# Kernel tuning notes

Measured on AMD Instinct MI355X. Metric: run time of the kernel, lower is better.

The kernel has to match this reference:

```python
import jax, jax.numpy as jnp
import numpy as np

B, C, H, W = 8, 64, 64, 64
T, G, HID = 8, 8, 64


def setup_inputs() -> dict:
    key = jax.random.key(0)
    ks = jax.random.split(key, 8)
    s = 0.05
    return {
        "h": jax.random.normal(ks[0], (B, C, H, W), jnp.float32),
        "w_in": jax.random.normal(ks[1], (G * T, C), jnp.float32) * s,
        "b_in": jnp.zeros((G * T,), jnp.float32),
        "w_ih": jax.random.normal(ks[2], (4 * HID, 1), jnp.float32) * s,
        "w_hh": jax.random.normal(ks[3], (4 * HID, HID), jnp.float32) * s,
        "b_ih": jnp.zeros((4 * HID,), jnp.float32),
        "b_hh": jnp.zeros((4 * HID,), jnp.float32),
        "w_s": jax.random.normal(ks[4], (1, HID), jnp.float32) * s,
        "b_s": jnp.zeros((1,), jnp.float32),
        "w_out": jax.random.normal(ks[5], (C, G * T), jnp.float32) * s,
        "b_out": jnp.zeros((C,), jnp.float32),
    }


def reference(h, w_in, b_in, w_ih, w_hh, b_ih, b_hh, w_s, b_s, w_out, b_out):
    Bb, Cc, Hh, Ww = h.shape
    # 1x1 conv in-projection: (B,C,H,W) -> (B,G*T,H,W)
    y = jnp.einsum('bchw,oc->bohw', h, w_in) + b_in[None, :, None, None]
    y = y.reshape(Bb, G, T, Hh, Ww)
    # (B,G,H,W,T) -> (N,T) scalar sequences
    seq = jnp.transpose(y, (0, 1, 3, 4, 2)).reshape(-1, T)
    N = seq.shape[0]
    xs = seq.T  # (T, N) time-major for scan
    bias = b_ih + b_hh  # (4H,)
    w_x = w_ih[:, 0]    # (4H,) scalar-input weights

    def step(carry, x_t):
        hprev, cprev = carry
        # gates: i, f, g, o in torch LSTM ordering
        gates = x_t[:, None] * w_x[None, :] + hprev @ w_hh.T + bias  # (N,4H)
        i, f, g, o = jnp.split(gates, 4, axis=1)
        i = jax.nn.sigmoid(i)
        f = jax.nn.sigmoid(f)
        o = jax.nn.sigmoid(o)
        g = jnp.tanh(g)
        c = f * cprev + i * g
        hn = o * jnp.tanh(c)
        s_t = hn @ w_s[0] + b_s[0]  # fused to_scalar: (N,)
        return (hn, c), s_t

    init = (jnp.zeros((N, HID), h.dtype), jnp.zeros((N, HID), h.dtype))
    _, s = jax.lax.scan(step, init, xs)  # s: (T, N)

    out = s.T.reshape(Bb, G, Hh, Ww, T)
    out = jnp.transpose(out, (0, 1, 4, 2, 3)).reshape(Bb, G * T, Hh, Ww)
    # 1x1 conv out-projection back to C channels
    out = jnp.einsum('bchw,oc->bohw', out, w_out) + b_out[None, :, None, None]
    return out
```

## Files before the change

### kernel.cpp

```cpp
#include <hip/hip_runtime.h>
#include <hip/hip_bf16.h>

#define HW    4096
#define BB    8
#define TT    8

constexpr int OFF_WFRAG = 0;
constexpr int OFF_WTOUT = OFF_WFRAG + 8704;
constexpr int OFF_WXB   = OFF_WTOUT + 4096;

constexpr float SI = -1.44269504088896340736f;
constexpr float SG =  2.88539008177792681472f;

typedef _Float16 halfx8 __attribute__((ext_vector_type(8)));
typedef float    floatx4 __attribute__((ext_vector_type(4)));
typedef float    floatx2 __attribute__((ext_vector_type(2)));

__device__ inline float fast_exp2(float x) {
#if __has_builtin(__builtin_amdgcn_exp2f)
    return __builtin_amdgcn_exp2f(x);
#else
    return __builtin_exp2f(x);
#endif
}
__device__ inline float fast_rcp(float x) {
#if __has_builtin(__builtin_amdgcn_rcpf)
    return __builtin_amdgcn_rcpf(x);
#else
    return 1.0f / x;
#endif
}
__device__ inline floatx2 exp2x2(floatx2 x) {
    floatx2 r; r.x = fast_exp2(x.x); r.y = fast_exp2(x.y); return r;
}
__device__ inline floatx2 rcpx2(floatx2 x) {
    floatx2 r; r.x = fast_rcp(x.x); r.y = fast_rcp(x.y); return r;
}

union pack8 { _Float16 h[8]; uint4 u; };

__global__ __launch_bounds__(256) void prep_kernel(
    const float* __restrict__ w_ih,  const float* __restrict__ w_hh,
    const float* __restrict__ b_ih,  const float* __restrict__ b_hh,
    const float* __restrict__ w_s,   const float* __restrict__ w_out,
    float* __restrict__ ws_f) {
    int tid = threadIdx.x;
    int bid = blockIdx.x;
    if (bid < 9) {
        int e = bid * 256 + tid;
        uint4* wf = (uint4*)(ws_f + OFF_WFRAG);
        if (e < 2048) {
            int l  = e & 63;
            int fi = e >> 6;
            int nb = fi >> 1, kc = fi & 1;
            int gate = (l & 15) + 16 * nb;
            int hid  = kc * 32 + (l >> 4) * 8;
            float sc = (gate >= 128 && gate < 192) ? SG : SI;
            const float* src = w_hh + gate * 64 + hid;
            pack8 p;
            #pragma unroll
            for (int j = 0; j < 8; ++j) p.h[j] = (_Float16)(src[j] * sc);
            wf[e] = p.u;
        } else if (e < 2176) {
            int t2 = e - 2048;
            int l = t2 & 63, kc = t2 >> 6;
            pack8 p;
            #pragma unroll
            for (int j = 0; j < 8; ++j) p.h[j] = (_Float16)0.0f;
            if ((l & 15) == 0) {
                #pragma unroll
                for (int j = 0; j < 8; ++j)
                    p.h[j] = (_Float16)w_s[kc * 32 + (l >> 4) * 8 + j];
            }
            wf[e] = p.u;
        }
    } else if (bid == 9) {
        floatx2* wxb = (floatx2*)(ws_f + OFF_WXB);
        float sc = (tid >= 128 && tid < 192) ? SG : SI;
        floatx2 v; v.x = w_ih[tid] * sc; v.y = (b_ih[tid] + b_hh[tid]) * sc;
        wxb[tid] = v;
    } else {
        #pragma unroll
        for (int i = 0; i < 8; ++i) {
            int idx = (bid - 10) * 2048 + tid + 256 * i;
            int o = idx & 63, c = idx >> 6;
            ws_f[OFF_WTOUT + idx] = w_out[o * 64 + c];
        }
    }
}

__global__ __launch_bounds__(512) void lstm_kernel(
    const float* __restrict__ hin,
    const float* __restrict__ ws_f,
    float* __restrict__ out,
    const float* __restrict__ w_in,
    const float* __restrict__ b_in,
    const float* __restrict__ b_s_p,
    const float* __restrict__ b_out) {
    __shared__ uint4 wfrag_lds[2176];
    __shared__ floatx2 wxb_lds[256];
    __shared__ __align__(16) float x_lds[1024];
    __shared__ __align__(16) _Float16 h_lds[9216];
    __shared__ __align__(16) float stile[1024];
    __shared__ __align__(16) float wt_lds[4096];

    int tid = threadIdx.x;
    int ptile = blockIdx.x & 255;
    int b     = blockIdx.x >> 8;
    int p0 = ptile * 16;

    int lane = tid & 63;
    int wv   = tid >> 6;
    int g    = wv;
    int s    = lane & 15;
    int q    = lane >> 4;

    const uint4* wfg = (const uint4*)(ws_f + OFF_WFRAG);
    #pragma unroll
    for (int i = 0; i < 5; ++i) {
        int e = tid + 512 * i;
        if (e < 2176) wfrag_lds[e] = wfg[e];
    }
    if (tid < 256) wxb_lds[tid] = ((const floatx2*)(ws_f + OFF_WXB))[tid];
    #pragma unroll
    for (int i = 0; i < 2; ++i)
        ((floatx4*)wt_lds)[tid + 512 * i] = ((const floatx4*)w_in)[tid + 512 * i];
    if (tid < 256) {
        int cc = tid >> 2, f4 = tid & 3;
        ((floatx4*)stile)[tid] = *(const floatx4*)&hin[(b * 64 + cc) * HW + p0 + f4 * 4];
    }
    __syncthreads();

    {
        floatx2 xacc; xacc.x = b_in[g * 8 + q]; xacc.y = b_in[g * 8 + q + 4];
        #pragma unroll 8
        for (int cc = 0; cc < 64; ++cc) {
            float hv = stile[cc * 16 + s];
            floatx2 w;
            w.x = wt_lds[(g * 8 + q) * 64 + cc];
            w.y = wt_lds[(g * 8 + q + 4) * 64 + cc];
            floatx2 h2; h2.x = hv; h2.y = hv;
            xacc = xacc + w * h2;
        }
        x_lds[g * 128 + q * 16 + s]       = xacc.x;
        x_lds[g * 128 + (q + 4) * 16 + s] = xacc.y;
    }
    #pragma unroll
    for (int i = 0; i < 9; ++i)
        ((unsigned*)h_lds)[tid + 512 * i] = 0u;
    __syncthreads();

    #pragma unroll
    for (int i = 0; i < 2; ++i)
        ((floatx4*)wt_lds)[tid + 512 * i] =
            ((const floatx4*)(ws_f + OFF_WTOUT))[tid + 512 * i];

    _Float16* hrow = h_lds + wv * 16 * 72;
    float bs = b_s_p[0];

    float c_st[4][4];
    #pragma unroll
    for (int hb = 0; hb < 4; ++hb)
        #pragma unroll
        for (int r = 0; r < 4; ++r) c_st[hb][r] = 0.0f;

    for (int t = 0; t < TT; ++t) {
        asm volatile("" ::: "memory");

        halfx8 a0 = *(const halfx8*)(hrow + s * 72 + q * 8);
        halfx8 a1 = *(const halfx8*)(hrow + s * 72 + q * 8 + 32);

        if (t > 0) {
            halfx8 sb0 = *(const halfx8*)&wfrag_lds[32 * 64 + lane];
            halfx8 sb1 = *(const halfx8*)&wfrag_lds[33 * 64 + lane];
            floatx4 sa = {0.f, 0.f, 0.f, 0.f};
            sa = __builtin_amdgcn_mfma_f32_16x16x32_f16(a0, sb0, sa, 0, 0, 0);
            sa = __builtin_amdgcn_mfma_f32_16x16x32_f16(a1, sb1, sa, 0, 0, 0);
            if (s == 0) {
                floatx4 o4 = {sa[0] + bs, sa[1] + bs, sa[2] + bs, sa[3] + bs};
                *(floatx4*)&stile[(g * 8 + (t - 1)) * 16 + q * 4] = o4;
            }
        }

        floatx4 xv = *(const floatx4*)&x_lds[g * 128 + t * 16 + q * 4];
        floatx2 xlo; xlo.x = xv[0]; xlo.y = xv[1];
        floatx2 xhi; xhi.x = xv[2]; xhi.y = xv[3];

        #pragma unroll
        for (int hb = 0; hb < 4; ++hb) {
            floatx4 acc[4];
            #pragma unroll
            for (int gi = 0; gi < 4; ++gi) {
                int nb = hb + 4 * gi;
                floatx2 wb = wxb_lds[s + 16 * nb];
                floatx2 lo = xlo * wb.x + wb.y;
                floatx2 hi = xhi * wb.x + wb.y;
                floatx4 a = {lo.x, lo.y, hi.x, hi.y};
                halfx8 b0 = *(const halfx8*)&wfrag_lds[(nb * 2 + 0) * 64 + lane];
                halfx8 b1 = *(const halfx8*)&wfrag_lds[(nb * 2 + 1) * 64 + lane];
                a = __builtin_amdgcn_mfma_f32_16x16x32_f16(a0, b0, a, 0, 0, 0);
                a = __builtin_amdgcn_mfma_f32_16x16x32_f16(a1, b1, a, 0, 0, 0);
                acc[gi] = a;
            }
            int s16 = s + 16 * hb;
            _Float16* wp = hrow + (q * 4) * 72 + s16;
            #pragma unroll
            for (int p = 0; p < 2; ++p) {
                int r0 = 2 * p;
                floatx2 Ei; Ei.x = fast_exp2(acc[0][r0]); Ei.y = fast_exp2(acc[0][r0 + 1]);
                floatx2 Ef; Ef.x = fast_exp2(acc[1][r0]); Ef.y = fast_exp2(acc[1][r0 + 1]);
                floatx2 Eg; Eg.x = fast_exp2(acc[2][r0]); Eg.y = fast_exp2(acc[2][r0 + 1]);
                floatx2 Eo; Eo.x = fast_exp2(acc[3][r0]); Eo.y = fast_exp2(acc[3][r0 + 1]);
                floatx2 Bf  = Ef + 1.0f;
                floatx2 Pig = (Ei + 1.0f) * (Eg + 1.0f);
                floatx2 cp; cp.x = c_st[hb][r0]; cp.y = c_st[hb][r0 + 1];
                floatx2 num = cp * Pig + (Eg * SG - SG) * Bf;
                floatx2 cs  = num * rcpx2(Bf * Pig);
                c_st[hb][r0] = cs.x; c_st[hb][r0 + 1] = cs.y;
                floatx2 Ec  = exp2x2(cs);
                floatx2 hn  = (Ec - 1.0f) * rcpx2((Eo + 1.0f) * (Ec + 1.0f));
                wp[(r0 + 0) * 72] = (_Float16)hn.x;
                wp[(r0 + 1) * 72] = (_Float16)hn.y;
            }
        }
    }
    {
        asm volatile("" ::: "memory");
        halfx8 a0 = *(const halfx8*)(hrow + s * 72 + q * 8);
        halfx8 a1 = *(const halfx8*)(hrow + s * 72 + q * 8 + 32);
        halfx8 sb0 = *(const halfx8*)&wfrag_lds[32 * 64 + lane];
        halfx8 sb1 = *(const halfx8*)&wfrag_lds[33 * 64 + lane];
        floatx4 sa = {0.f, 0.f, 0.f, 0.f};
        sa = __builtin_amdgcn_mfma_f32_16x16x32_f16(a0, sb0, sa, 0, 0, 0);
        sa = __builtin_amdgcn_mfma_f32_16x16x32_f16(a1, sb1, sa, 0, 0, 0);
        if (s == 0) {
            floatx4 o4 = {sa[0] + bs, sa[1] + bs, sa[2] + bs, sa[3] + bs};
            *(floatx4*)&stile[(g * 8 + 7) * 16 + q * 4] = o4;
        }
    }
    __syncthreads();

    {
        int px = tid & 15;
        int oo = tid >> 4;
        floatx2 acc; acc.x = b_out[oo]; acc.y = b_out[oo + 32];
        #pragma unroll 8
        for (int c = 0; c < 64; ++c) {
            float sv = stile[c * 16 + px];
            floatx2 w;
            w.x = wt_lds[c * 64 + oo];
            w.y = wt_lds[c * 64 + oo + 32];
            floatx2 s2; s2.x = sv; s2.y = sv;
            acc = acc + w * s2;
        }
        out[(b * 64 + oo) * HW + p0 + px]      = acc.x;
        out[(b * 64 + oo + 32) * HW + p0 + px] = acc.y;
    }
}

extern "C" void kernel_launch(void* const* d_in, const int* in_sizes, int n_in,
                              void* d_out, int out_size, void* d_ws, size_t ws_size,
                              hipStream_t stream) {
    const float* h     = (const float*)d_in[0];
    const float* w_in  = (const float*)d_in[1];
    const float* b_in  = (const float*)d_in[2];
    const float* w_ih  = (const float*)d_in[3];
    const float* w_hh  = (const float*)d_in[4];
    const float* b_ih  = (const float*)d_in[5];
    const float* b_hh  = (const float*)d_in[6];
    const float* w_s   = (const float*)d_in[7];
    const float* b_s   = (const float*)d_in[8];
    const float* w_out = (const float*)d_in[9];
    const float* b_out = (const float*)d_in[10];
    float* out = (float*)d_out;
    float* ws  = (float*)d_ws;

    prep_kernel<<<12, 256, 0, stream>>>(w_ih, w_hh, b_ih, b_hh, w_s, w_out, ws);
    lstm_kernel<<<2048, 512, 0, stream>>>(h, ws, out, w_in, b_in, b_s, b_out);
}
```

Before: 232.7 us.

## Permute LSTM gate layout for packed h stores, hoist weights, vectorize out-projection

The recurrent weight fragments and input/bias table are permuted in the prep kernel so that each lane owns four consecutive hidden units. The new h state can then be written to LDS as halfx4 vectors instead of scalar half stores. The per-gate input weights and the to_scalar fragments are hoisted into registers outside the time loop. The out-projection now reads w_out untransposed with floatx4 LDS loads, which removes the transpose pass from the prep kernel. A min-blocks launch bound is added; it may force a tight register budget and cause spills, given the extra register-resident weights.

```diff
diff --git a/kernel.cpp b/kernel.cpp
--- a/kernel.cpp
+++ b/kernel.cpp
@@ -6,13 +6,13 @@
 #define TT    8
 
 constexpr int OFF_WFRAG = 0;
-constexpr int OFF_WTOUT = OFF_WFRAG + 8704;
-constexpr int OFF_WXB   = OFF_WTOUT + 4096;
+constexpr int OFF_WXB   = 12800;
 
 constexpr float SI = -1.44269504088896340736f;
 constexpr float SG =  2.88539008177792681472f;
 
 typedef _Float16 halfx8 __attribute__((ext_vector_type(8)));
+typedef _Float16 halfx4 __attribute__((ext_vector_type(4)));
 typedef float    floatx4 __attribute__((ext_vector_type(4)));
 typedef float    floatx2 __attribute__((ext_vector_type(2)));
 
@@ -53,9 +53,10 @@
             int l  = e & 63;
             int fi = e >> 6;
             int nb = fi >> 1, kc = fi & 1;
-            int gate = (l & 15) + 16 * nb;
+            int hb = nb & 3, gi = nb >> 2;
+            int gate = gi * 64 + 4 * (l & 15) + hb;
             int hid  = kc * 32 + (l >> 4) * 8;
-            float sc = (gate >= 128 && gate < 192) ? SG : SI;
+            float sc = (gi == 2) ? SG : SI;
             const float* src = w_hh + gate * 64 + hid;
             pack8 p;
             #pragma unroll
@@ -74,29 +75,24 @@
             }
             wf[e] = p.u;
         }
-    } else if (bid == 9) {
-        floatx2* wxb = (floatx2*)(ws_f + OFF_WXB);
-        float sc = (tid >= 128 && tid < 192) ? SG : SI;
-        floatx2 v; v.x = w_ih[tid] * sc; v.y = (b_ih[tid] + b_hh[tid]) * sc;
-        wxb[tid] = v;
     } else {
-        #pragma unroll
-        for (int i = 0; i < 8; ++i) {
-            int idx = (bid - 10) * 2048 + tid + 256 * i;
-            int o = idx & 63, c = idx >> 6;
-            ws_f[OFF_WTOUT + idx] = w_out[o * 64 + c];
-        }
-    }
-}
-
-__global__ __launch_bounds__(512) void lstm_kernel(
+        int s_ = tid & 15, hb = (tid >> 4) & 3, gi = tid >> 6;
+        int gate = gi * 64 + 4 * s_ + hb;
+        float sc = (gi == 2) ? SG : SI;
+        floatx2 v; v.x = w_ih[gate] * sc; v.y = (b_ih[gate] + b_hh[gate]) * sc;
+        ((floatx2*)(ws_f + OFF_WXB))[tid] = v;
+    }
+}
+
+__global__ __launch_bounds__(512, 4) void lstm_kernel(
     const float* __restrict__ hin,
     const float* __restrict__ ws_f,
     float* __restrict__ out,
     const float* __restrict__ w_in,
     const float* __restrict__ b_in,
     const float* __restrict__ b_s_p,
-    const float* __restrict__ b_out) {
+    const float* __restrict__ b_out,
+    const float* __restrict__ w_out) {
     __shared__ uint4 wfrag_lds[2176];
     __shared__ floatx2 wxb_lds[256];
     __shared__ __align__(16) float x_lds[1024];
@@ -152,8 +148,13 @@
 
     #pragma unroll
     for (int i = 0; i < 2; ++i)
-        ((floatx4*)wt_lds)[tid + 512 * i] =
-            ((const floatx4*)(ws_f + OFF_WTOUT))[tid + 512 * i];
+        ((floatx4*)wt_lds)[tid + 512 * i] = ((const floatx4*)w_out)[tid + 512 * i];
+
+    floatx2 wbr[16];
+    #pragma unroll
+    for (int nb = 0; nb < 16; ++nb) wbr[nb] = wxb_lds[s + 16 * nb];
+    halfx8 sb0 = *(const halfx8*)&wfrag_lds[32 * 64 + lane];
+    halfx8 sb1 = *(const halfx8*)&wfrag_lds[33 * 64 + lane];
 
     _Float16* hrow = h_lds + wv * 16 * 72;
     float bs = b_s_p[0];
@@ -171,8 +172,6 @@
         halfx8 a1 = *(const halfx8*)(hrow + s * 72 + q * 8 + 32);
 
         if (t > 0) {
-            halfx8 sb0 = *(const halfx8*)&wfrag_lds[32 * 64 + lane];
-            halfx8 sb1 = *(const halfx8*)&wfrag_lds[33 * 64 + lane];
             floatx4 sa = {0.f, 0.f, 0.f, 0.f};
             sa = __builtin_amdgcn_mfma_f32_16x16x32_f16(a0, sb0, sa, 0, 0, 0);
             sa = __builtin_amdgcn_mfma_f32_16x16x32_f16(a1, sb1, sa, 0, 0, 0);
@@ -186,13 +185,15 @@
         floatx2 xlo; xlo.x = xv[0]; xlo.y = xv[1];
         floatx2 xhi; xhi.x = xv[2]; xhi.y = xv[3];
 
+        halfx4 hpack[4];
+
         #pragma unroll
         for (int hb = 0; hb < 4; ++hb) {
             floatx4 acc[4];
             #pragma unroll
             for (int gi = 0; gi < 4; ++gi) {
                 int nb = hb + 4 * gi;
-                floatx2 wb = wxb_lds[s + 16 * nb];
+                floatx2 wb = wbr[nb];
                 floatx2 lo = xlo * wb.x + wb.y;
                 floatx2 hi = xhi * wb.x + wb.y;
                 floatx4 a = {lo.x, lo.y, hi.x, hi.y};
@@ -202,8 +203,6 @@
                 a = __builtin_amdgcn_mfma_f32_16x16x32_f16(a1, b1, a, 0, 0, 0);
                 acc[gi] = a;
             }
-            int s16 = s + 16 * hb;
-            _Float16* wp = hrow + (q * 4) * 72 + s16;
             #pragma unroll
             for (int p = 0; p < 2; ++p) {
                 int r0 = 2 * p;
@@ -219,17 +218,22 @@
                 c_st[hb][r0] = cs.x; c_st[hb][r0 + 1] = cs.y;
                 floatx2 Ec  = exp2x2(cs);
                 floatx2 hn  = (Ec - 1.0f) * rcpx2((Eo + 1.0f) * (Ec + 1.0f));
-                wp[(r0 + 0) * 72] = (_Float16)hn.x;
-                wp[(r0 + 1) * 72] = (_Float16)hn.y;
-            }
+                hpack[r0 + 0][hb] = (_Float16)hn.x;
+                hpack[r0 + 1][hb] = (_Float16)hn.y;
+            }
+        }
+        {
+            _Float16* wp = hrow + (q * 4) * 72 + 4 * s;
+            *(halfx4*)(wp +   0) = hpack[0];
+            *(halfx4*)(wp +  72) = hpack[1];
+            *(halfx4*)(wp + 144) = hpack[2];
+            *(halfx4*)(wp + 216) = hpack[3];
         }
     }
     {
         asm volatile("" ::: "memory");
         halfx8 a0 = *(const halfx8*)(hrow + s * 72 + q * 8);
         halfx8 a1 = *(const halfx8*)(hrow + s * 72 + q * 8 + 32);
-        halfx8 sb0 = *(const halfx8*)&wfrag_lds[32 * 64 + lane];
-        halfx8 sb1 = *(const halfx8*)&wfrag_lds[33 * 64 + lane];
         floatx4 sa = {0.f, 0.f, 0.f, 0.f};
         sa = __builtin_amdgcn_mfma_f32_16x16x32_f16(a0, sb0, sa, 0, 0, 0);
         sa = __builtin_amdgcn_mfma_f32_16x16x32_f16(a1, sb1, sa, 0, 0, 0);
@@ -244,14 +248,16 @@
         int px = tid & 15;
         int oo = tid >> 4;
         floatx2 acc; acc.x = b_out[oo]; acc.y = b_out[oo + 32];
-        #pragma unroll 8
-        for (int c = 0; c < 64; ++c) {
-            float sv = stile[c * 16 + px];
-            floatx2 w;
-            w.x = wt_lds[c * 64 + oo];
-            w.y = wt_lds[c * 64 + oo + 32];
-            floatx2 s2; s2.x = sv; s2.y = sv;
-            acc = acc + w * s2;
+        #pragma unroll
+        for (int c4 = 0; c4 < 16; ++c4) {
+            floatx4 w0 = *(const floatx4*)&wt_lds[oo * 64 + c4 * 4];
+            floatx4 w1 = *(const floatx4*)&wt_lds[(oo + 32) * 64 + c4 * 4];
+            #pragma unroll
+            for (int j = 0; j < 4; ++j) {
+                float sv = stile[(c4 * 4 + j) * 16 + px];
+                acc.x += w0[j] * sv;
+                acc.y += w1[j] * sv;
+            }
         }
         out[(b * 64 + oo) * HW + p0 + px]      = acc.x;
         out[(b * 64 + oo + 32) * HW + p0 + px] = acc.y;
@@ -275,6 +281,6 @@
     float* out = (float*)d_out;
     float* ws  = (float*)d_ws;
 
-    prep_kernel<<<12, 256, 0, stream>>>(w_ih, w_hh, b_ih, b_hh, w_s, w_out, ws);
-    lstm_kernel<<<2048, 512, 0, stream>>>(h, ws, out, w_in, b_in, b_s, b_out);
-}
+    prep_kernel<<<10, 256, 0, stream>>>(w_ih, w_hh, b_ih, b_hh, w_s, w_out, ws);
+    lstm_kernel<<<2048, 512, 0, stream>>>(h, ws, out, w_in, b_in, b_s, b_out, w_out);
+}
```

New measurement: 481.5 us. +106.9%, slower.
